# Optimization experiments

Measured on AMD Instinct MI355X. Metric: run time of the kernel, lower is better.

Reference implementation:

```python
import jax, jax.numpy as jnp
import numpy as np

N_NODES = 100000
N_EDGES = 3200000
VM, VA, PG, QG, PD, QD = 0, 1, 2, 3, 4, 5
G, B = 0, 1


def setup_inputs() -> dict:
    key = jax.random.key(0)
    k1, k2, k3, k4, k5 = jax.random.split(key, 5)
    pred = jax.random.normal(k1, (N_NODES, 6), dtype=jnp.float32)
    target = jax.random.normal(k2, (N_NODES, 6), dtype=jnp.float32)
    edge_index = jax.random.randint(k3, (2, N_EDGES), 0, N_NODES, dtype=jnp.int64)
    edge_attr = jax.random.normal(k4, (N_EDGES, 2), dtype=jnp.float32)
    mask = jax.random.randint(k5, (N_NODES, 6), 0, 2) == 1
    return {"pred": pred, "target": target, "edge_index": edge_index,
            "edge_attr": edge_attr, "mask": mask}


def reference(pred, target, edge_index, edge_attr, mask):
    # temp_pred[~mask] = target[~mask]
    temp_pred = jnp.where(mask, pred, target)
    vm = temp_pred[:, VM]
    va = temp_pred[:, VA]
    pg = temp_pred[:, PG]
    qg = temp_pred[:, QG]
    pd = temp_pred[:, PD]
    qd = temp_pred[:, QD]
    g = edge_attr[:, G]
    b = edge_attr[:, B]
    src, dst = edge_index[0], edge_index[1]

    v_from = vm[src]                      # [E] gather
    v_to = vm[dst]
    ang = va[src] - va[dst]
    c, s = jnp.cos(ang), jnp.sin(ang)
    vv = v_from * v_to
    p_flow = vv * (g * c + b * s)         # [E]
    q_flow = vv * (g * s - b * c)

    # scatter-add flows into source nodes
    p_calc = jax.ops.segment_sum(p_flow, src, num_segments=N_NODES)
    q_calc = jax.ops.segment_sum(q_flow, src, num_segments=N_NODES)

    p_imb = pg - pd - p_calc
    q_imb = qg - qd - q_calc
    loss = jnp.mean(p_imb ** 2) + jnp.mean(q_imb ** 2)
    return loss
```

## Files before the change

### kernel.cpp

```cpp
#include <hip/hip_runtime.h>
#include <cstdint>

#define N_NODES 100000
#define N_EDGES 3200000
#define SPAN    256
#define SHIFT   8
#define NB      ((N_NODES + SPAN - 1) / SPAN)
#define CHUNK   4096
#define BTH     512
#define NITER   (CHUNK / BTH)
#define NBLK    ((N_EDGES + CHUNK - 1) / CHUNK)
#define PREF_W  (NB + 1)

__global__ __launch_bounds__(256)
void prep_kernel(const float* __restrict__ pred,
                 const float* __restrict__ target,
                 const void* __restrict__ mask,
                 float2* __restrict__ u_tab,
                 float2* __restrict__ base_pq,
                 float* __restrict__ d_out, int out_size) {
    __shared__ int s_mask8;
    if (threadIdx.x < 64) {
        uint32_t w = ((const uint32_t*)mask)[threadIdx.x];
        bool nz = (w & 0xFFFFFF00u) != 0u;
        unsigned long long m = __ballot(nz);
        if (threadIdx.x == 0) s_mask8 = (m != 0ull) ? 1 : 0;
    }
    if (blockIdx.x == 0 && threadIdx.x == 0)
        for (int k = 0; k < out_size; ++k) d_out[k] = 0.0f;
    __syncthreads();

    int i = blockIdx.x * 256 + threadIdx.x;
    if (i >= N_NODES) return;

    const float2* p2 = (const float2*)pred;
    const float2* t2 = (const float2*)target;
    float2 pa = p2[3 * i], pb = p2[3 * i + 1], pc = p2[3 * i + 2];
    float2 ta = t2[3 * i], tb = t2[3 * i + 1], tc = t2[3 * i + 2];
    float pr[6] = {pa.x, pa.y, pb.x, pb.y, pc.x, pc.y};
    float tg[6] = {ta.x, ta.y, tb.x, tb.y, tc.x, tc.y};
    int mk[6];
    if (s_mask8) {
        const uint16_t* mu = (const uint16_t*)mask;
        uint16_t m0 = mu[3 * i], m1 = mu[3 * i + 1], m2 = mu[3 * i + 2];
        mk[0] = m0 & 0xFF; mk[1] = m0 >> 8;
        mk[2] = m1 & 0xFF; mk[3] = m1 >> 8;
        mk[4] = m2 & 0xFF; mk[5] = m2 >> 8;
    } else {
        const int2* mi = (const int2*)mask;
        int2 m0 = mi[3 * i], m1 = mi[3 * i + 1], m2 = mi[3 * i + 2];
        mk[0] = m0.x; mk[1] = m0.y; mk[2] = m1.x;
        mk[3] = m1.y; mk[4] = m2.x; mk[5] = m2.y;
    }
    float tp[6];
    #pragma unroll
    for (int j = 0; j < 6; ++j) tp[j] = mk[j] ? pr[j] : tg[j];

    float s, c;
    sincosf(tp[1], &s, &c);
    u_tab[i]   = make_float2(tp[0] * c, tp[0] * s);
    base_pq[i] = make_float2(tp[2] - tp[4], tp[3] - tp[5]);
}

__global__ __launch_bounds__(BTH)
void bin_kernel(const void* __restrict__ edge_index,
                const float2* __restrict__ edge_attr,
                const float2* __restrict__ u_tab,
                uint2* __restrict__ recs,
                uint32_t* __restrict__ pref) {
    __shared__ uint2 s_rec[CHUNK];
    __shared__ uint32_t s_cnt[NB];
    __shared__ uint32_t s_pref[PREF_W];
    __shared__ uint32_t s_wsum[8], s_woff[8];
    __shared__ int s_i64;

    const int tid = threadIdx.x;
    const int lane = tid & 63, wid = tid >> 6;
    if (tid < 64) {
        uint32_t w = ((const uint32_t*)edge_index)[tid];
        bool nz = (tid & 1) && (w != 0u);
        unsigned long long m = __ballot(nz);
        if (tid == 0) s_i64 = (m == 0ull) ? 1 : 0;
    }
    if (tid < NB) s_cnt[tid] = 0u;
    __syncthreads();
    const bool is64 = (s_i64 != 0);
    const int ebase = blockIdx.x * CHUNK;
    const int nE = min(CHUNK, N_EDGES - ebase);

    uint32_t src_r[NITER];
    #pragma unroll
    for (int it = 0; it < NITER; ++it) {
        int j = it * BTH + tid;
        uint32_t s = 0u;
        if (j < nE) {
            int e = ebase + j;
            s = is64 ? (uint32_t)((const unsigned long long*)edge_index)[e]
                     : ((const uint32_t*)edge_index)[e];
            atomicAdd(&s_cnt[s >> SHIFT], 1u);
        }
        src_r[it] = s;
    }
    __syncthreads();

    {
        uint32_t v0 = (tid < NB) ? s_cnt[tid] : 0u;
        uint32_t x = v0;
        #pragma unroll
        for (int off = 1; off < 64; off <<= 1) {
            uint32_t y = (uint32_t)__shfl_up((int)x, off, 64);
            if (lane >= off) x += y;
        }
        if (lane == 63) s_wsum[wid] = x;
        __syncthreads();
        if (tid < 8) {
            uint32_t w0 = s_wsum[tid];
            uint32_t xx = w0;
            #pragma unroll
            for (int off = 1; off < 8; off <<= 1) {
                uint32_t y = (uint32_t)__shfl_up((int)xx, off, 64);
                if (tid >= off) xx += y;
            }
            s_woff[tid] = xx - w0;
        }
        __syncthreads();
        uint32_t incl = x + s_woff[wid];
        if (tid < NB) s_pref[tid + 1] = incl;
        if (tid == 0) s_pref[0] = 0u;
        if (tid < NB) s_cnt[tid] = 0u;
        __syncthreads();
    }

    #pragma unroll
    for (int it = 0; it < NITER; ++it) {
        int j = it * BTH + tid;
        if (j < nE) {
            int e = ebase + j;
            uint32_t dst = is64
                ? (uint32_t)((const unsigned long long*)edge_index)[(size_t)N_EDGES + e]
                : ((const uint32_t*)edge_index)[(size_t)N_EDGES + e];
            float2 gb = edge_attr[e];
            float2 u  = u_tab[dst];
            float vr = gb.x * u.x - gb.y * u.y;
            float vi = -(gb.y * u.x + gb.x * u.y);
            uint32_t nid = src_r[it];
            uint32_t bk = nid >> SHIFT, lid = nid & (SPAN - 1);
            uint32_t r = atomicAdd(&s_cnt[bk], 1u);
            uint2 rc;
            rc.x = (__float_as_uint(vr) & ~0xFFu) | lid;
            rc.y = __float_as_uint(vi);
            s_rec[s_pref[bk] + r] = rc;
        }
    }
    __syncthreads();

    {
        const uint4* s4 = (const uint4*)s_rec;
        uint4* a4 = (uint4*)(recs + (size_t)blockIdx.x * CHUNK);
        for (int k = tid; k < nE / 2; k += BTH) a4[k] = s4[k];
        if ((nE & 1) && tid == 0)
            recs[(size_t)blockIdx.x * CHUNK + nE - 1] = s_rec[nE - 1];
    }
    for (int b = tid; b < PREF_W; b += BTH)
        pref[(size_t)blockIdx.x * PREF_W + b] = s_pref[b];
}

__global__ __launch_bounds__(1024)
void reduce_kernel(const uint2* __restrict__ recs,
                   const uint32_t* __restrict__ pref,
                   const float2* __restrict__ u_tab,
                   const float2* __restrict__ base_pq,
                   float* __restrict__ d_out) {
    __shared__ float2 s_acc[4][SPAN];
    __shared__ float s_part[16];
    if (threadIdx.x < SPAN) {
        #pragma unroll
        for (int r = 0; r < 4; ++r) s_acc[r][threadIdx.x] = make_float2(0.0f, 0.0f);
    }
    __syncthreads();

    const int b = blockIdx.x;
    const int rep = (threadIdx.x >> 6) & 3;
    if (threadIdx.x < NBLK) {
        const uint32_t* prow = pref + (size_t)threadIdx.x * PREF_W;
        uint32_t s = prow[b], e = prow[b + 1];
        const uint2* arena = recs + (size_t)threadIdx.x * CHUNK;
        for (uint32_t j = s; j < e; ++j) {
            uint2 rc = arena[j];
            uint32_t lid = rc.x & 0xFFu;
            atomicAdd(&s_acc[rep][lid].x, __uint_as_float(rc.x & ~0xFFu));
            atomicAdd(&s_acc[rep][lid].y, __uint_as_float(rc.y));
        }
    }
    __syncthreads();

    float v = 0.0f;
    int node = b * SPAN + (int)threadIdx.x;
    if (threadIdx.x < SPAN && node < N_NODES) {
        float2 S = make_float2(0.0f, 0.0f);
        #pragma unroll
        for (int rr = 0; rr < 4; ++rr) {
            float2 t = s_acc[rr][threadIdx.x];
            S.x += t.x; S.y += t.y;
        }
        float2 ui = u_tab[node];
        float2 bp = base_pq[node];
        float pc = ui.x * S.x - ui.y * S.y;
        float qc = ui.x * S.y + ui.y * S.x;
        float p = bp.x - pc, q = bp.y - qc;
        v = p * p + q * q;
    }
    #pragma unroll
    for (int off = 32; off > 0; off >>= 1) v += __shfl_down(v, off, 64);
    if ((threadIdx.x & 63) == 0) s_part[threadIdx.x >> 6] = v;
    __syncthreads();
    if (threadIdx.x == 0) {
        float t = 0.0f;
        #pragma unroll
        for (int w = 0; w < 16; ++w) t += s_part[w];
        atomicAdd(d_out, t * (1.0f / (float)N_NODES));
    }
}

extern "C" void kernel_launch(void* const* d_in, const int* in_sizes, int n_in,
                              void* d_out, int out_size, void* d_ws, size_t ws_size,
                              hipStream_t stream) {
    const float*  pred       = (const float*)d_in[0];
    const float*  target     = (const float*)d_in[1];
    const void*   edge_index = d_in[2];
    const float2* edge_attr  = (const float2*)d_in[3];
    const void*   mask       = d_in[4];
    float* out = (float*)d_out;

    char* ws = (char*)d_ws;
    float2*   u_tab   = (float2*)ws;
    float2*   base_pq = (float2*)(ws + 800000);
    uint32_t* pref    = (uint32_t*)(ws + 1600000);
    uint2*    recs    = (uint2*)(ws + 2826176);

    prep_kernel<<<(N_NODES + 255) / 256, 256, 0, stream>>>(
        pred, target, mask, u_tab, base_pq, out, out_size);

    bin_kernel<<<NBLK, BTH, 0, stream>>>(
        edge_index, edge_attr, u_tab, recs, pref);

    reduce_kernel<<<NB, 1024, 0, stream>>>(
        recs, pref, u_tab, base_pq, out);
}
```

Measured before the change: 173.2 us.

## Fuse prep, binning and reduction into one cooperative persistent kernel with global sort

```diff
diff --git a/kernel.cpp b/kernel.cpp
--- a/kernel.cpp
+++ b/kernel.cpp
@@ -1,100 +1,103 @@
 #include <hip/hip_runtime.h>
+#include <hip/hip_cooperative_groups.h>
 #include <cstdint>
+
+namespace cg = cooperative_groups;
 
 #define N_NODES 100000
 #define N_EDGES 3200000
 #define SPAN    256
 #define SHIFT   8
-#define NB      ((N_NODES + SPAN - 1) / SPAN)
-#define CHUNK   4096
-#define BTH     512
-#define NITER   (CHUNK / BTH)
-#define NBLK    ((N_EDGES + CHUNK - 1) / CHUNK)
+#define NB      391
+#define NBLK    256
+#define BTH     1024
+#define CHUNK   12500
+#define NITER   13
 #define PREF_W  (NB + 1)
 
-__global__ __launch_bounds__(256)
-void prep_kernel(const float* __restrict__ pred,
-                 const float* __restrict__ target,
-                 const void* __restrict__ mask,
-                 float2* __restrict__ u_tab,
-                 float2* __restrict__ base_pq,
-                 float* __restrict__ d_out, int out_size) {
-    __shared__ int s_mask8;
-    if (threadIdx.x < 64) {
-        uint32_t w = ((const uint32_t*)mask)[threadIdx.x];
-        bool nz = (w & 0xFFFFFF00u) != 0u;
-        unsigned long long m = __ballot(nz);
-        if (threadIdx.x == 0) s_mask8 = (m != 0ull) ? 1 : 0;
-    }
-    if (blockIdx.x == 0 && threadIdx.x == 0)
-        for (int k = 0; k < out_size; ++k) d_out[k] = 0.0f;
-    __syncthreads();
-
-    int i = blockIdx.x * 256 + threadIdx.x;
-    if (i >= N_NODES) return;
-
-    const float2* p2 = (const float2*)pred;
-    const float2* t2 = (const float2*)target;
-    float2 pa = p2[3 * i], pb = p2[3 * i + 1], pc = p2[3 * i + 2];
-    float2 ta = t2[3 * i], tb = t2[3 * i + 1], tc = t2[3 * i + 2];
-    float pr[6] = {pa.x, pa.y, pb.x, pb.y, pc.x, pc.y};
-    float tg[6] = {ta.x, ta.y, tb.x, tb.y, tc.x, tc.y};
-    int mk[6];
-    if (s_mask8) {
-        const uint16_t* mu = (const uint16_t*)mask;
-        uint16_t m0 = mu[3 * i], m1 = mu[3 * i + 1], m2 = mu[3 * i + 2];
-        mk[0] = m0 & 0xFF; mk[1] = m0 >> 8;
-        mk[2] = m1 & 0xFF; mk[3] = m1 >> 8;
-        mk[4] = m2 & 0xFF; mk[5] = m2 >> 8;
-    } else {
-        const int2* mi = (const int2*)mask;
-        int2 m0 = mi[3 * i], m1 = mi[3 * i + 1], m2 = mi[3 * i + 2];
-        mk[0] = m0.x; mk[1] = m0.y; mk[2] = m1.x;
-        mk[3] = m1.y; mk[4] = m2.x; mk[5] = m2.y;
-    }
-    float tp[6];
-    #pragma unroll
-    for (int j = 0; j < 6; ++j) tp[j] = mk[j] ? pr[j] : tg[j];
-
-    float s, c;
-    sincosf(tp[1], &s, &c);
-    u_tab[i]   = make_float2(tp[0] * c, tp[0] * s);
-    base_pq[i] = make_float2(tp[2] - tp[4], tp[3] - tp[5]);
-}
-
 __global__ __launch_bounds__(BTH)
-void bin_kernel(const void* __restrict__ edge_index,
-                const float2* __restrict__ edge_attr,
-                const float2* __restrict__ u_tab,
-                uint2* __restrict__ recs,
-                uint32_t* __restrict__ pref) {
+void fused_kernel(const float* __restrict__ pred,
+                  const float* __restrict__ target,
+                  const void* __restrict__ edge_index,
+                  const float2* __restrict__ edge_attr,
+                  const void* __restrict__ mask,
+                  float2* __restrict__ u_tab,
+                  float2* __restrict__ base_pq,
+                  uint16_t* __restrict__ prefT,
+                  uint32_t* __restrict__ base_gT,
+                  uint2* __restrict__ gsorted,
+                  float* __restrict__ d_out, int out_size) {
     __shared__ uint2 s_rec[CHUNK];
     __shared__ uint32_t s_cnt[NB];
     __shared__ uint32_t s_pref[PREF_W];
-    __shared__ uint32_t s_wsum[8], s_woff[8];
-    __shared__ int s_i64;
-
+    __shared__ uint32_t s_wsum[16], s_woff[16];
+    __shared__ float2 s_acc[4][SPAN];
+    __shared__ float s_part[4];
+    __shared__ uint32_t s_tS[2], s_tN[2];
+    __shared__ int s_mask8, s_i64;
+
+    cg::grid_group grid = cg::this_grid();
     const int tid = threadIdx.x;
     const int lane = tid & 63, wid = tid >> 6;
+    const int blk = blockIdx.x;
+
     if (tid < 64) {
-        uint32_t w = ((const uint32_t*)edge_index)[tid];
-        bool nz = (tid & 1) && (w != 0u);
-        unsigned long long m = __ballot(nz);
-        if (tid == 0) s_i64 = (m == 0ull) ? 1 : 0;
-    }
-    if (tid < NB) s_cnt[tid] = 0u;
+        uint32_t w  = ((const uint32_t*)mask)[tid];
+        uint32_t w2 = ((const uint32_t*)edge_index)[tid];
+        unsigned long long mA = __ballot((w & 0xFFFFFF00u) != 0u);
+        unsigned long long mB = __ballot((tid & 1) && (w2 != 0u));
+        if (tid == 0) { s_mask8 = (mA != 0ull); s_i64 = (mB == 0ull); }
+    }
+    if (blk == 0 && tid == 0)
+        for (int k = 0; k < out_size; ++k) d_out[k] = 0.0f;
+    __syncthreads();
+
+    {
+        int i = blk * BTH + tid;
+        if (i < N_NODES) {
+            const float2* p2 = (const float2*)pred;
+            const float2* t2 = (const float2*)target;
+            float2 pa = p2[3 * i], pb = p2[3 * i + 1], pc = p2[3 * i + 2];
+            float2 ta = t2[3 * i], tb = t2[3 * i + 1], tc = t2[3 * i + 2];
+            float pr[6] = {pa.x, pa.y, pb.x, pb.y, pc.x, pc.y};
+            float tg[6] = {ta.x, ta.y, tb.x, tb.y, tc.x, tc.y};
+            int mk[6];
+            if (s_mask8) {
+                const uint16_t* mu = (const uint16_t*)mask;
+                uint16_t m0 = mu[3 * i], m1 = mu[3 * i + 1], m2 = mu[3 * i + 2];
+                mk[0] = m0 & 0xFF; mk[1] = m0 >> 8;
+                mk[2] = m1 & 0xFF; mk[3] = m1 >> 8;
+                mk[4] = m2 & 0xFF; mk[5] = m2 >> 8;
+            } else {
+                const int2* mi = (const int2*)mask;
+                int2 m0 = mi[3 * i], m1 = mi[3 * i + 1], m2 = mi[3 * i + 2];
+                mk[0] = m0.x; mk[1] = m0.y; mk[2] = m1.x;
+                mk[3] = m1.y; mk[4] = m2.x; mk[5] = m2.y;
+            }
+            float tp[6];
+            #pragma unroll
+            for (int j = 0; j < 6; ++j) tp[j] = mk[j] ? pr[j] : tg[j];
+            float s, c;
+            sincosf(tp[1], &s, &c);
+            u_tab[i]   = make_float2(tp[0] * c, tp[0] * s);
+            base_pq[i] = make_float2(tp[2] - tp[4], tp[3] - tp[5]);
+        }
+    }
+    __threadfence();
+    grid.sync();
+
+    for (int b = tid; b < NB; b += BTH) s_cnt[b] = 0u;
     __syncthreads();
     const bool is64 = (s_i64 != 0);
-    const int ebase = blockIdx.x * CHUNK;
-    const int nE = min(CHUNK, N_EDGES - ebase);
+    const long long ebase = (long long)blk * CHUNK;
 
     uint32_t src_r[NITER];
     #pragma unroll
     for (int it = 0; it < NITER; ++it) {
         int j = it * BTH + tid;
         uint32_t s = 0u;
-        if (j < nE) {
-            int e = ebase + j;
+        if (j < CHUNK) {
+            long long e = ebase + j;
             s = is64 ? (uint32_t)((const unsigned long long*)edge_index)[e]
                      : ((const uint32_t*)edge_index)[e];
             atomicAdd(&s_cnt[s >> SHIFT], 1u);
@@ -113,11 +116,11 @@
         }
         if (lane == 63) s_wsum[wid] = x;
         __syncthreads();
-        if (tid < 8) {
+        if (tid < 16) {
             uint32_t w0 = s_wsum[tid];
             uint32_t xx = w0;
             #pragma unroll
-            for (int off = 1; off < 8; off <<= 1) {
+            for (int off = 1; off < 16; off <<= 1) {
                 uint32_t y = (uint32_t)__shfl_up((int)xx, off, 64);
                 if (tid >= off) xx += y;
             }
@@ -134,8 +137,8 @@
     #pragma unroll
     for (int it = 0; it < NITER; ++it) {
         int j = it * BTH + tid;
-        if (j < nE) {
-            int e = ebase + j;
+        if (j < CHUNK) {
+            long long e = ebase + j;
             uint32_t dst = is64
                 ? (uint32_t)((const unsigned long long*)edge_index)[(size_t)N_EDGES + e]
                 : ((const uint32_t*)edge_index)[(size_t)N_EDGES + e];
@@ -148,77 +151,110 @@
             uint32_t r = atomicAdd(&s_cnt[bk], 1u);
             uint2 rc;
             rc.x = (__float_as_uint(vr) & ~0xFFu) | lid;
-            rc.y = __float_as_uint(vi);
+            rc.y = (__float_as_uint(vi) & ~0x1FFu) | bk;
             s_rec[s_pref[bk] + r] = rc;
         }
     }
     __syncthreads();
-
-    {
-        const uint4* s4 = (const uint4*)s_rec;
-        uint4* a4 = (uint4*)(recs + (size_t)blockIdx.x * CHUNK);
-        for (int k = tid; k < nE / 2; k += BTH) a4[k] = s4[k];
-        if ((nE & 1) && tid == 0)
-            recs[(size_t)blockIdx.x * CHUNK + nE - 1] = s_rec[nE - 1];
-    }
     for (int b = tid; b < PREF_W; b += BTH)
-        pref[(size_t)blockIdx.x * PREF_W + b] = s_pref[b];
-}
-
-__global__ __launch_bounds__(1024)
-void reduce_kernel(const uint2* __restrict__ recs,
-                   const uint32_t* __restrict__ pref,
-                   const float2* __restrict__ u_tab,
-                   const float2* __restrict__ base_pq,
-                   float* __restrict__ d_out) {
-    __shared__ float2 s_acc[4][SPAN];
-    __shared__ float s_part[16];
-    if (threadIdx.x < SPAN) {
-        #pragma unroll
-        for (int r = 0; r < 4; ++r) s_acc[r][threadIdx.x] = make_float2(0.0f, 0.0f);
-    }
-    __syncthreads();
-
-    const int b = blockIdx.x;
-    const int rep = (threadIdx.x >> 6) & 3;
-    if (threadIdx.x < NBLK) {
-        const uint32_t* prow = pref + (size_t)threadIdx.x * PREF_W;
-        uint32_t s = prow[b], e = prow[b + 1];
-        const uint2* arena = recs + (size_t)threadIdx.x * CHUNK;
-        for (uint32_t j = s; j < e; ++j) {
-            uint2 rc = arena[j];
-            uint32_t lid = rc.x & 0xFFu;
-            atomicAdd(&s_acc[rep][lid].x, __uint_as_float(rc.x & ~0xFFu));
-            atomicAdd(&s_acc[rep][lid].y, __uint_as_float(rc.y));
-        }
-    }
-    __syncthreads();
-
-    float v = 0.0f;
-    int node = b * SPAN + (int)threadIdx.x;
-    if (threadIdx.x < SPAN && node < N_NODES) {
-        float2 S = make_float2(0.0f, 0.0f);
-        #pragma unroll
-        for (int rr = 0; rr < 4; ++rr) {
-            float2 t = s_acc[rr][threadIdx.x];
-            S.x += t.x; S.y += t.y;
-        }
-        float2 ui = u_tab[node];
-        float2 bp = base_pq[node];
-        float pc = ui.x * S.x - ui.y * S.y;
-        float qc = ui.x * S.y + ui.y * S.x;
-        float p = bp.x - pc, q = bp.y - qc;
-        v = p * p + q * q;
-    }
-    #pragma unroll
-    for (int off = 32; off > 0; off >>= 1) v += __shfl_down(v, off, 64);
-    if ((threadIdx.x & 63) == 0) s_part[threadIdx.x >> 6] = v;
-    __syncthreads();
-    if (threadIdx.x == 0) {
-        float t = 0.0f;
-        #pragma unroll
-        for (int w = 0; w < 16; ++w) t += s_part[w];
-        atomicAdd(d_out, t * (1.0f / (float)N_NODES));
+        prefT[(size_t)b * NBLK + blk] = (uint16_t)s_pref[b];
+    __threadfence();
+    grid.sync();
+
+    {
+        int nt = 0;
+        for (int b = blk; b < NB; b += NBLK) {
+            uint32_t lo = 0, cnt = 0;
+            if (tid < NBLK) {
+                lo  = prefT[(size_t)b * NBLK + tid];
+                cnt = (uint32_t)prefT[(size_t)(b + 1) * NBLK + tid] - lo;
+            }
+            uint32_t x = cnt;
+            #pragma unroll
+            for (int off = 1; off < 64; off <<= 1) {
+                uint32_t y = (uint32_t)__shfl_up((int)x, off, 64);
+                if (lane >= off) x += y;
+            }
+            uint32_t ls = lo;
+            #pragma unroll
+            for (int off = 32; off > 0; off >>= 1)
+                ls += (uint32_t)__shfl_down((int)ls, off, 64);
+            if (tid < NBLK && lane == 63) s_wsum[wid] = x;
+            if (tid < NBLK && lane == 0)  s_wsum[8 + wid] = ls;
+            __syncthreads();
+            if (tid == 0) {
+                uint32_t S = s_wsum[8] + s_wsum[9] + s_wsum[10] + s_wsum[11];
+                uint32_t c0 = s_wsum[0], c1 = s_wsum[1], c2 = s_wsum[2];
+                s_woff[0] = 0u; s_woff[1] = c0; s_woff[2] = c0 + c1;
+                s_woff[3] = c0 + c1 + c2;
+                s_tS[nt] = S;
+                s_tN[nt] = c0 + c1 + c2 + s_wsum[3];
+            }
+            __syncthreads();
+            if (tid < NBLK)
+                base_gT[(size_t)tid * NB + b] = s_tS[nt] + s_woff[wid] + (x - cnt);
+            __syncthreads();
+            ++nt;
+        }
+    }
+    __threadfence();
+    grid.sync();
+
+    for (int b = tid; b < NB; b += BTH)
+        s_cnt[b] = base_gT[(size_t)blk * NB + b];
+    __syncthreads();
+    for (int slot = tid; slot < CHUNK; slot += BTH) {
+        uint2 rc = s_rec[slot];
+        uint32_t bk = rc.y & 0x1FFu;
+        uint32_t pos = s_cnt[bk] + ((uint32_t)slot - s_pref[bk]);
+        gsorted[pos] = rc;
+    }
+    __threadfence();
+    grid.sync();
+
+    {
+        float loss = 0.0f;
+        int nt = 0;
+        for (int b = blk; b < NB; b += NBLK) {
+            if (tid < SPAN) {
+                #pragma unroll
+                for (int r = 0; r < 4; ++r) s_acc[r][tid] = make_float2(0.f, 0.f);
+            }
+            __syncthreads();
+            const uint32_t S = s_tS[nt], n = s_tN[nt];
+            const int rep = wid & 3;
+            for (uint32_t k = tid; k < n; k += BTH) {
+                uint2 rc = gsorted[S + k];
+                uint32_t lid = rc.x & 0xFFu;
+                atomicAdd(&s_acc[rep][lid].x, __uint_as_float(rc.x & ~0xFFu));
+                atomicAdd(&s_acc[rep][lid].y, __uint_as_float(rc.y & ~0x1FFu));
+            }
+            __syncthreads();
+            float v = 0.0f;
+            int node = b * SPAN + tid;
+            if (tid < SPAN && node < N_NODES) {
+                float2 Sm = make_float2(0.f, 0.f);
+                #pragma unroll
+                for (int rr = 0; rr < 4; ++rr) {
+                    float2 t = s_acc[rr][tid];
+                    Sm.x += t.x; Sm.y += t.y;
+                }
+                float2 ui = u_tab[node];
+                float2 bp = base_pq[node];
+                float pc = ui.x * Sm.x - ui.y * Sm.y;
+                float qc = ui.x * Sm.y + ui.y * Sm.x;
+                float p = bp.x - pc, q = bp.y - qc;
+                v = p * p + q * q;
+            }
+            #pragma unroll
+            for (int off = 32; off > 0; off >>= 1) v += __shfl_down(v, off, 64);
+            if (tid < SPAN && lane == 0) s_part[wid] = v;
+            __syncthreads();
+            if (tid == 0) loss += s_part[0] + s_part[1] + s_part[2] + s_part[3];
+            __syncthreads();
+            ++nt;
+        }
+        if (tid == 0) atomicAdd(d_out, loss * (1.0f / (float)N_NODES));
     }
 }
 
@@ -235,15 +271,16 @@
     char* ws = (char*)d_ws;
     float2*   u_tab   = (float2*)ws;
     float2*   base_pq = (float2*)(ws + 800000);
-    uint32_t* pref    = (uint32_t*)(ws + 1600000);
-    uint2*    recs    = (uint2*)(ws + 2826176);
-
-    prep_kernel<<<(N_NODES + 255) / 256, 256, 0, stream>>>(
-        pred, target, mask, u_tab, base_pq, out, out_size);
-
-    bin_kernel<<<NBLK, BTH, 0, stream>>>(
-        edge_index, edge_attr, u_tab, recs, pref);
-
-    reduce_kernel<<<NB, 1024, 0, stream>>>(
-        recs, pref, u_tab, base_pq, out);
+    uint16_t* prefT   = (uint16_t*)(ws + 1600000);
+    uint32_t* base_gT = (uint32_t*)(ws + 1800704);
+    uint2*    gsorted = (uint2*)(ws + 2201088);
+
+    int out_size_v = out_size;
+    void* args[] = {
+        (void*)&pred, (void*)&target, (void*)&edge_index, (void*)&edge_attr,
+        (void*)&mask, (void*)&u_tab, (void*)&base_pq, (void*)&prefT,
+        (void*)&base_gT, (void*)&gsorted, (void*)&out, (void*)&out_size_v
+    };
+    hipLaunchCooperativeKernel((void*)fused_kernel, dim3(NBLK), dim3(BTH),
+                               args, 0, stream);
 }
```

Result: slower. 663.8 us (+283.3%).
